# Kernel optimization log

Hardware: AMD Instinct MI355X
Metric: run time of the kernel (lower is better)

## Reference

```python
import jax, jax.numpy as jnp
import numpy as np


def _dct_last(x):
    # torch_dct along last axis: mirror-extend, forward-normalized FFT, sign(Re)*|X|
    L = x.shape[-1]
    arr = jnp.concatenate([x, x[..., ::-1]], axis=-1)
    X = jnp.fft.fft(arr, axis=-1, norm='forward')[..., :L]
    return jnp.abs(X) * jnp.sign(X.real)


def _dct_2d(x):
    row = _dct_last(x)
    col = _dct_last(jnp.swapaxes(row, -1, -2))
    return jnp.swapaxes(col, -1, -2)


def _dct_chan(x):
    # same transform along channel dim (axis 1)
    C = x.shape[1]
    arr = jnp.concatenate([x, x[:, ::-1]], axis=1)
    X = jnp.fft.fft(arr, axis=1, norm='forward')[:, :C]
    return jnp.abs(X) * jnp.sign(X.real)


def _idct_chan(x):
    # iDCT_Channel: shifted double-length spectrum -> ifft -> flipped real part
    B, C, H, W = x.shape
    v = jnp.arange(2 * C)
    shift = jnp.exp((-1j * 2.0 * jnp.pi * (C - 0.5) / (2 * C)) * v).astype(jnp.complex64)
    vi = x * (2.0 * C)
    flipneg = -vi[:, 1:][:, ::-1]                     # -flip(x[:,1:])
    full = jnp.concatenate([vi, jnp.zeros((B, 1, H, W), x.dtype), flipneg], axis=1)
    full = full.astype(jnp.complex64) * shift[None, :, None, None]
    xx = jnp.fft.ifft(full, axis=1)
    return xx[:, :C][:, ::-1].real


TOPK = 8
TOPK_CHANS = 8


def setup_inputs() -> dict:
    key = jax.random.key(0)
    k1, k2, k3, k4 = jax.random.split(key, 4)
    B, C, H, W = 4, 64, 256, 256
    red = 8
    return {
        'ip': jax.random.normal(k1, (B, C, H, W), dtype=jnp.float32),
        'fc1_w': jax.random.normal(k2, (C // red, C * TOPK), dtype=jnp.float32) * (1.0 / np.sqrt(C * TOPK)),
        'fc2_w': jax.random.normal(k3, (C, C // red), dtype=jnp.float32) * (1.0 / np.sqrt(C // red)),
        'conv_w': jax.random.normal(k4, (1, TOPK_CHANS, 3, 3), dtype=jnp.float32) * (1.0 / np.sqrt(TOPK_CHANS * 9)),
        'conv_b': jnp.zeros((1,), dtype=jnp.float32),
    }


def reference(ip, fc1_w, fc2_w, conv_w, conv_b):
    ip = ip.astype(jnp.float32)
    # channel-frequency attention
    ca = _dct_chan(ip)                                        # [B,C,H,W]
    ct = jnp.transpose(ca, (0, 2, 3, 1))                      # [B,H,W,C]
    topv = jax.lax.top_k(ct, TOPK_CHANS)[0]                   # [B,H,W,k]
    channel_topk = jnp.transpose(topv, (0, 3, 1, 2))          # [B,k,H,W]
    conv = jax.lax.conv_general_dilated(
        channel_topk, conv_w, (1, 1), 'SAME',
        dimension_numbers=('NCHW', 'OIHW', 'NCHW')) + conv_b[None, :, None, None]
    gate = jax.nn.sigmoid(conv)                               # [B,1,H,W]
    final = ca * gate
    x = _idct_chan(final).astype(jnp.float32)                 # [B,C,H,W]
    # spatial-DCT top-k channel gating MLP
    B, C = x.shape[0], x.shape[1]
    dct2 = _dct_2d(x).reshape(B, C, -1)                       # [B,C,H*W]
    topc = jax.lax.top_k(dct2, TOPK)[0].reshape(B, -1)        # [B,C*topk]
    h = jax.nn.relu(topc @ fc1_w.T)                           # [B,C//red]
    w = jax.nn.sigmoid(h @ fc2_w.T).reshape(B, C, 1, 1)       # [B,C,1,1]
    return x * w
```

## Files before the change

### kernel.cpp

```cpp
#include <hip/hip_runtime.h>
#include <hip/hip_bf16.h>
#include <math.h>

#define HW 65536
#define NCH 64
#define NB 4

typedef __attribute__((ext_vector_type(8))) short bf16x8;
typedef __attribute__((ext_vector_type(4))) float f32x4;
typedef __attribute__((ext_vector_type(8))) unsigned short u16x8;

__device__ inline unsigned short f2b(float f) {
  __hip_bfloat16 h = __float2bfloat16(f);
  return *(unsigned short*)&h;
}

__global__ void gen_tables(float* __restrict__ Mc, float* __restrict__ Nc,
                           unsigned short* __restrict__ Tb) {
  int i = blockIdx.x * 256 + threadIdx.x;
  const double PI = 3.14159265358979323846;
  if (i < 4096) {
    int k = i >> 6, c = i & 63;
    Mc[i] = (float)(cos(PI * (double)(k * (2 * c + 1)) / 128.0) / 64.0);
    Nc[i] = (c == 0) ? 1.0f
                     : (float)(2.0 * cos(PI * (double)(c * (2 * k + 1)) / 128.0));
  }
  {
    int n = i >> 8, k = i & 255;
    float v = (float)(cos(PI * (double)(n * (2 * k + 1)) / 512.0) / 256.0);
    Tb[i] = f2b(v);
  }
}

__global__ __launch_bounds__(256) void gemm64(
    const float* __restrict__ Ag, int lda, long long sAb,
    const float* __restrict__ Bg, int ldb, long long sBb,
    float* __restrict__ Cg, int ldc, long long sCb, int K,
    const float* __restrict__ gate, long long sGb) {
  __shared__ float As[16][68];
  __shared__ float Bs[16][68];
  const int tid = threadIdx.x;
  const int tx = tid & 15, ty = tid >> 4;
  const int bn = blockIdx.x, bm = blockIdx.y, bz = blockIdx.z;
  const float* Ab = Ag + bz * sAb + (long long)bm * 64 * lda;
  const float* Bp = Bg + bz * sBb;
  const long long n0 = (long long)bn * 64;
  const int bcol = tid & 63;
  const int brow = tid >> 6;
  const int acol = tid & 15;
  const int arow = tid >> 4;
  float g = 1.0f;
  if (gate) g = gate[bz * sGb + n0 + bcol];
  float acc[4][4] = {{0.f}};

  for (int k0 = 0; k0 < K; k0 += 16) {
#pragma unroll
    for (int i = 0; i < 4; i++) {
      int r = arow + 16 * i;
      As[acol][r] = Ab[(long long)r * lda + (k0 + acol)];
    }
#pragma unroll
    for (int i = 0; i < 4; i++) {
      int r = brow + 4 * i;
      Bs[r][bcol] = Bp[(long long)(k0 + r) * ldb + n0 + bcol] * g;
    }
    __syncthreads();
#pragma unroll
    for (int kk = 0; kk < 16; kk++) {
      float4 a4 = *(const float4*)&As[kk][ty * 4];
      float4 b4 = *(const float4*)&Bs[kk][tx * 4];
      float a[4] = {a4.x, a4.y, a4.z, a4.w};
      float b[4] = {b4.x, b4.y, b4.z, b4.w};
#pragma unroll
      for (int i = 0; i < 4; i++)
#pragma unroll
        for (int j = 0; j < 4; j++) acc[i][j] = fmaf(a[i], b[j], acc[i][j]);
    }
    __syncthreads();
  }
#pragma unroll
  for (int i = 0; i < 4; i++) {
    float4 o;
    o.x = acc[i][0]; o.y = acc[i][1]; o.z = acc[i][2]; o.w = acc[i][3];
    *(float4*)&Cg[bz * sCb + (long long)(bm * 64 + ty * 4 + i) * ldc + n0 +
                  tx * 4] = o;
  }
}

__global__ __launch_bounds__(256) void mfma_rowdct(
    const float* __restrict__ x, const unsigned short* __restrict__ Tb,
    unsigned short* __restrict__ Rt) {
  __shared__ unsigned short As[128][40];
  __shared__ unsigned short Bs[128][40];
  const int tid = threadIdx.x;
  const int m0 = blockIdx.y * 128;
  const int n0 = blockIdx.x * 128;
  const int wv = tid >> 6, lane = tid & 63;
  const int wr = wv >> 1, wc = wv & 1;
  const int l15 = lane & 15, kb = lane >> 4;
  const int srow = tid & 127, sseg = tid >> 7;
  f32x4 acc[4][4] = {};

  for (int k0 = 0; k0 < 256; k0 += 32) {
    {
      const float* p = x + (long long)(m0 + srow) * 256 + k0 + sseg * 8;
      float4 v0 = *(const float4*)p;
      float4 v1 = *(const float4*)(p + 4);
      u16x8 w;
      w[0] = f2b(v0.x); w[1] = f2b(v0.y); w[2] = f2b(v0.z); w[3] = f2b(v0.w);
      w[4] = f2b(v1.x); w[5] = f2b(v1.y); w[6] = f2b(v1.z); w[7] = f2b(v1.w);
      *(u16x8*)&As[srow][sseg * 8] = w;
    }
    *(u16x8*)&Bs[srow][sseg * 8] =
        *(const u16x8*)(Tb + (n0 + srow) * 256 + k0 + sseg * 8);
    __syncthreads();
    bf16x8 a[4], b[4];
#pragma unroll
    for (int mi = 0; mi < 4; mi++)
      a[mi] = *(const bf16x8*)&As[wr * 64 + mi * 16 + l15][kb * 8];
#pragma unroll
    for (int ni = 0; ni < 4; ni++)
      b[ni] = *(const bf16x8*)&Bs[wc * 64 + ni * 16 + l15][kb * 8];
#pragma unroll
    for (int mi = 0; mi < 4; mi++)
#pragma unroll
      for (int ni = 0; ni < 4; ni++)
        acc[mi][ni] = __builtin_amdgcn_mfma_f32_16x16x32_bf16(
            a[mi], b[ni], acc[mi][ni], 0, 0, 0);
    __syncthreads();
  }

  const int img = m0 >> 8;
  const int hb = (m0 & 255) + wr * 64 + kb * 4;
#pragma unroll
  for (int mi = 0; mi < 4; mi++) {
#pragma unroll
    for (int ni = 0; ni < 4; ni++) {
      int h = hb + mi * 16;
      int n = n0 + wc * 64 + ni * 16 + l15;
      ushort4 o;
      o.x = f2b(acc[mi][ni][0]); o.y = f2b(acc[mi][ni][1]);
      o.z = f2b(acc[mi][ni][2]); o.w = f2b(acc[mi][ni][3]);
      *(ushort4*)&Rt[(long long)img * 65536 + (long long)n * 256 + h] = o;
    }
  }
}

__global__ __launch_bounds__(256) void mfma_coldct_top8(
    const unsigned short* __restrict__ Tb, const unsigned short* __restrict__ Rt,
    float* __restrict__ top8out) {
  __shared__ unsigned short As[128][40];
  __shared__ unsigned short Bs[128][40];
  __shared__ float lists[256 * 8];
  const int tid = threadIdx.x;
  const int m0 = blockIdx.y * 128;
  const int n0 = blockIdx.x * 128;
  const int img = blockIdx.z;
  const int wv = tid >> 6, lane = tid & 63;
  const int wr = wv >> 1, wc = wv & 1;
  const int l15 = lane & 15, kb = lane >> 4;
  const int srow = tid & 127, sseg = tid >> 7;
  const unsigned short* Rb = Rt + (long long)img * 65536;
  f32x4 acc[4][4] = {};

  for (int k0 = 0; k0 < 256; k0 += 32) {
    *(u16x8*)&As[srow][sseg * 8] =
        *(const u16x8*)(Tb + (m0 + srow) * 256 + k0 + sseg * 8);
    *(u16x8*)&Bs[srow][sseg * 8] =
        *(const u16x8*)(Rb + (n0 + srow) * 256 + k0 + sseg * 8);
    __syncthreads();
    bf16x8 a[4], b[4];
#pragma unroll
    for (int mi = 0; mi < 4; mi++)
      a[mi] = *(const bf16x8*)&As[wr * 64 + mi * 16 + l15][kb * 8];
#pragma unroll
    for (int ni = 0; ni < 4; ni++)
      b[ni] = *(const bf16x8*)&Bs[wc * 64 + ni * 16 + l15][kb * 8];
#pragma unroll
    for (int mi = 0; mi < 4; mi++)
#pragma unroll
      for (int ni = 0; ni < 4; ni++)
        acc[mi][ni] = __builtin_amdgcn_mfma_f32_16x16x32_bf16(
            a[mi], b[ni], acc[mi][ni], 0, 0, 0);
    __syncthreads();
  }

  float t[8];
#pragma unroll
  for (int j = 0; j < 8; j++) t[j] = -INFINITY;
#pragma unroll
  for (int mi = 0; mi < 4; mi++)
#pragma unroll
    for (int ni = 0; ni < 4; ni++)
#pragma unroll
      for (int j = 0; j < 4; j++) {
        float v = acc[mi][ni][j];
#pragma unroll
        for (int q = 0; q < 8; q++) {
          if (v > t[q]) { float tmp = t[q]; t[q] = v; v = tmp; }
        }
      }
#pragma unroll
  for (int j = 0; j < 8; j++) lists[tid * 8 + j] = t[j];
  __syncthreads();
  for (int s = 128; s >= 1; s >>= 1) {
    if (tid < s) {
      int ii = 0, jj = 0;
      float out[8];
#pragma unroll
      for (int m = 0; m < 8; m++) {
        float av = lists[tid * 8 + ii];
        float bv = lists[(tid + s) * 8 + jj];
        bool ta = (av >= bv);
        out[m] = ta ? av : bv;
        ii += ta ? 1 : 0;
        jj += ta ? 0 : 1;
      }
#pragma unroll
      for (int m = 0; m < 8; m++) lists[tid * 8 + m] = out[m];
    }
    __syncthreads();
  }
  if (tid < 8) {
    long long idx = ((long long)img * gridDim.y + blockIdx.y) * gridDim.x +
                    blockIdx.x;
    top8out[idx * 8 + tid] = lists[tid];
  }
}

__global__ __launch_bounds__(256) void top8_chan(const float* __restrict__ ca,
                                                 float* __restrict__ ct) {
  int gidx = blockIdx.x * 256 + threadIdx.x;
  int b = gidx >> 16, p = gidx & 65535;
  const float* src = ca + (long long)b * NCH * HW + p;
  float t[8];
#pragma unroll
  for (int j = 0; j < 8; j++) t[j] = -INFINITY;
  for (int c = 0; c < NCH; c++) {
    float v = src[(long long)c * HW];
#pragma unroll
    for (int q = 0; q < 8; q++) {
      if (v > t[q]) { float tmp = t[q]; t[q] = v; v = tmp; }
    }
  }
  float* dst = ct + (long long)b * 8 * HW + p;
#pragma unroll
  for (int j = 0; j < 8; j++) dst[(long long)j * HW] = t[j];
}

__global__ __launch_bounds__(256) void conv_gate(const float* __restrict__ ct,
                                                 const float* __restrict__ cw,
                                                 const float* __restrict__ cbias,
                                                 float* __restrict__ gate) {
  int gidx = blockIdx.x * 256 + threadIdx.x;
  int b = gidx >> 16, p = gidx & 65535;
  int h = p >> 8, w = p & 255;
  float acc = cbias[0];
#pragma unroll
  for (int j = 0; j < 8; j++) {
    const float* base = ct + ((long long)b * 8 + j) * HW;
#pragma unroll
    for (int dy = 0; dy < 3; dy++) {
      int y = h + dy - 1;
      if ((unsigned)y < 256u) {
#pragma unroll
        for (int dx = 0; dx < 3; dx++) {
          int x = w + dx - 1;
          if ((unsigned)x < 256u)
            acc += base[y * 256 + x] * cw[j * 9 + dy * 3 + dx];
        }
      }
    }
  }
  gate[gidx] = 1.0f / (1.0f + expf(-acc));
}

__global__ void merge_top8(const float* __restrict__ lists,
                           float* __restrict__ topc) {
  int img = blockIdx.x * 64 + threadIdx.x;
  if (img >= 256) return;
  float t[8];
#pragma unroll
  for (int j = 0; j < 8; j++) t[j] = -INFINITY;
  for (int l = 0; l < 4; l++) {
#pragma unroll
    for (int m = 0; m < 8; m++) {
      float v = lists[(img * 4 + l) * 8 + m];
#pragma unroll
      for (int q = 0; q < 8; q++) {
        if (v > t[q]) { float tmp = t[q]; t[q] = v; v = tmp; }
      }
    }
  }
  int b = img >> 6, c = img & 63;
#pragma unroll
  for (int j = 0; j < 8; j++) topc[b * 512 + c * 8 + j] = t[j];
}

__global__ void mlp_kernel(const float* __restrict__ topc,
                           const float* __restrict__ fc1,
                           const float* __restrict__ fc2,
                           float* __restrict__ wout) {
  __shared__ float hbuf[32];
  int tid = threadIdx.x;
  if (tid < 32) {
    int b = tid >> 3, i = tid & 7;
    float acc = 0.f;
    for (int j = 0; j < 512; j++) acc += topc[b * 512 + j] * fc1[i * 512 + j];
    hbuf[tid] = fmaxf(acc, 0.f);
  }
  __syncthreads();
  int b = tid >> 6, c = tid & 63;
  float acc = 0.f;
#pragma unroll
  for (int i = 0; i < 8; i++) acc += hbuf[b * 8 + i] * fc2[c * 8 + i];
  wout[tid] = 1.0f / (1.0f + expf(-acc));
}

__global__ __launch_bounds__(256) void scale_out(float* __restrict__ out,
                                                 const float* __restrict__ wout) {
  long long i = ((long long)blockIdx.x * 256 + threadIdx.x) * 4;
  float4 v = *(float4*)&out[i];
  float s = wout[(int)(i >> 16)];
  v.x *= s; v.y *= s; v.z *= s; v.w *= s;
  *(float4*)&out[i] = v;
}

extern "C" void kernel_launch(void* const* d_in, const int* in_sizes, int n_in,
                              void* d_out, int out_size, void* d_ws,
                              size_t ws_size, hipStream_t stream) {
  (void)in_sizes; (void)n_in; (void)out_size; (void)ws_size;
  const float* ip  = (const float*)d_in[0];
  const float* fc1 = (const float*)d_in[1];
  const float* fc2 = (const float*)d_in[2];
  const float* cw  = (const float*)d_in[3];
  const float* cb  = (const float*)d_in[4];
  float* out = (float*)d_out;
  float* ws = (float*)d_ws;

  float* Mc     = ws;
  float* Nc     = ws + 4096;
  unsigned short* Tb = (unsigned short*)(ws + 8192);
  float* gateb  = ws + 139264;
  float* wfin   = ws + 401408;
  float* topc   = ws + 401664;
  float* listsb = ws + 403712;
  float* ca     = ws + 1048576;
  float* ct8    = ws + 1048576 + 16777216;

  const long long CHW = (long long)NCH * HW;

  gen_tables<<<256, 256, 0, stream>>>(Mc, Nc, Tb);

  gemm64<<<dim3(1024, 1, 4), 256, 0, stream>>>(
      Mc, 64, 0, ip, HW, CHW, ca, HW, CHW, 64, nullptr, 0);

  top8_chan<<<1024, 256, 0, stream>>>(ca, ct8);
  conv_gate<<<1024, 256, 0, stream>>>(ct8, cw, cb, gateb);

  gemm64<<<dim3(1024, 1, 4), 256, 0, stream>>>(
      Nc, 64, 0, ca, HW, CHW, out, HW, CHW, 64, gateb, HW);

  unsigned short* Rt = (unsigned short*)ca;
  mfma_rowdct<<<dim3(2, 512), 256, 0, stream>>>(out, Tb, Rt);

  mfma_coldct_top8<<<dim3(2, 2, 256), 256, 0, stream>>>(Tb, Rt, listsb);

  merge_top8<<<4, 64, 0, stream>>>(listsb, topc);
  mlp_kernel<<<1, 256, 0, stream>>>(topc, fc1, fc2, wfin);
  scale_out<<<16384, 256, 0, stream>>>(out, wfin);
}
```

Before: 321.0 us.

## Eliminate inverse channel DCT by applying gate directly to input

Because the channel gate depends only on (b,h,w), the inverse channel DCT of the gated spectrum reduces to the original input times the gate. The second 64x64 channel GEMM and its table are therefore removed. The gate multiply is folded into the row-DCT load and into the final scaling kernel, which now reads the input and gate instead of a stored intermediate. This saves a full read and write pass over the tensor. It relies on the forward and inverse transforms being exact inverses, treating abs times sign of the real part as equal to the real part.

```diff
diff --git a/kernel.cpp b/kernel.cpp
--- a/kernel.cpp
+++ b/kernel.cpp
@@ -15,15 +15,13 @@
   return *(unsigned short*)&h;
 }
 
-__global__ void gen_tables(float* __restrict__ Mc, float* __restrict__ Nc,
+__global__ void gen_tables(float* __restrict__ Mc,
                            unsigned short* __restrict__ Tb) {
   int i = blockIdx.x * 256 + threadIdx.x;
   const double PI = 3.14159265358979323846;
   if (i < 4096) {
     int k = i >> 6, c = i & 63;
     Mc[i] = (float)(cos(PI * (double)(k * (2 * c + 1)) / 128.0) / 64.0);
-    Nc[i] = (c == 0) ? 1.0f
-                     : (float)(2.0 * cos(PI * (double)(c * (2 * k + 1)) / 128.0));
   }
   {
     int n = i >> 8, k = i & 255;
@@ -87,9 +85,56 @@
   }
 }
 
+__global__ __launch_bounds__(256) void top8_chan(const float* __restrict__ ca,
+                                                 float* __restrict__ ct) {
+  int gidx = blockIdx.x * 256 + threadIdx.x;
+  int b = gidx >> 16, p = gidx & 65535;
+  const float* src = ca + (long long)b * NCH * HW + p;
+  float t[8];
+#pragma unroll
+  for (int j = 0; j < 8; j++) t[j] = -INFINITY;
+  for (int c = 0; c < NCH; c++) {
+    float v = src[(long long)c * HW];
+#pragma unroll
+    for (int q = 0; q < 8; q++) {
+      if (v > t[q]) { float tmp = t[q]; t[q] = v; v = tmp; }
+    }
+  }
+  float* dst = ct + (long long)b * 8 * HW + p;
+#pragma unroll
+  for (int j = 0; j < 8; j++) dst[(long long)j * HW] = t[j];
+}
+
+__global__ __launch_bounds__(256) void conv_gate(const float* __restrict__ ct,
+                                                 const float* __restrict__ cw,
+                                                 const float* __restrict__ cbias,
+                                                 float* __restrict__ gate) {
+  int gidx = blockIdx.x * 256 + threadIdx.x;
+  int b = gidx >> 16, p = gidx & 65535;
+  int h = p >> 8, w = p & 255;
+  float acc = cbias[0];
+#pragma unroll
+  for (int j = 0; j < 8; j++) {
+    const float* base = ct + ((long long)b * 8 + j) * HW;
+#pragma unroll
+    for (int dy = 0; dy < 3; dy++) {
+      int y = h + dy - 1;
+      if ((unsigned)y < 256u) {
+#pragma unroll
+        for (int dx = 0; dx < 3; dx++) {
+          int x = w + dx - 1;
+          if ((unsigned)x < 256u)
+            acc += base[y * 256 + x] * cw[j * 9 + dy * 3 + dx];
+        }
+      }
+    }
+  }
+  gate[gidx] = 1.0f / (1.0f + expf(-acc));
+}
+
 __global__ __launch_bounds__(256) void mfma_rowdct(
-    const float* __restrict__ x, const unsigned short* __restrict__ Tb,
-    unsigned short* __restrict__ Rt) {
+    const float* __restrict__ ip, const float* __restrict__ gateb,
+    const unsigned short* __restrict__ Tb, unsigned short* __restrict__ Rt) {
   __shared__ unsigned short As[128][40];
   __shared__ unsigned short Bs[128][40];
   const int tid = threadIdx.x;
@@ -103,12 +148,18 @@
 
   for (int k0 = 0; k0 < 256; k0 += 32) {
     {
-      const float* p = x + (long long)(m0 + srow) * 256 + k0 + sseg * 8;
-      float4 v0 = *(const float4*)p;
-      float4 v1 = *(const float4*)(p + 4);
+      const int r = m0 + srow;
+      const int h = r & 255;
+      const int b = r >> 14;
+      const float* p  = ip + (long long)r * 256 + k0 + sseg * 8;
+      const float* gp = gateb + ((long long)b << 16) + (h << 8) + k0 + sseg * 8;
+      float4 v0 = *(const float4*)p,  v1 = *(const float4*)(p + 4);
+      float4 g0 = *(const float4*)gp, g1 = *(const float4*)(gp + 4);
       u16x8 w;
-      w[0] = f2b(v0.x); w[1] = f2b(v0.y); w[2] = f2b(v0.z); w[3] = f2b(v0.w);
-      w[4] = f2b(v1.x); w[5] = f2b(v1.y); w[6] = f2b(v1.z); w[7] = f2b(v1.w);
+      w[0] = f2b(v0.x * g0.x); w[1] = f2b(v0.y * g0.y);
+      w[2] = f2b(v0.z * g0.z); w[3] = f2b(v0.w * g0.w);
+      w[4] = f2b(v1.x * g1.x); w[5] = f2b(v1.y * g1.y);
+      w[6] = f2b(v1.z * g1.z); w[7] = f2b(v1.w * g1.w);
       *(u16x8*)&As[srow][sseg * 8] = w;
     }
     *(u16x8*)&Bs[srow][sseg * 8] =
@@ -228,53 +279,6 @@
   }
 }
 
-__global__ __launch_bounds__(256) void top8_chan(const float* __restrict__ ca,
-                                                 float* __restrict__ ct) {
-  int gidx = blockIdx.x * 256 + threadIdx.x;
-  int b = gidx >> 16, p = gidx & 65535;
-  const float* src = ca + (long long)b * NCH * HW + p;
-  float t[8];
-#pragma unroll
-  for (int j = 0; j < 8; j++) t[j] = -INFINITY;
-  for (int c = 0; c < NCH; c++) {
-    float v = src[(long long)c * HW];
-#pragma unroll
-    for (int q = 0; q < 8; q++) {
-      if (v > t[q]) { float tmp = t[q]; t[q] = v; v = tmp; }
-    }
-  }
-  float* dst = ct + (long long)b * 8 * HW + p;
-#pragma unroll
-  for (int j = 0; j < 8; j++) dst[(long long)j * HW] = t[j];
-}
-
-__global__ __launch_bounds__(256) void conv_gate(const float* __restrict__ ct,
-                                                 const float* __restrict__ cw,
-                                                 const float* __restrict__ cbias,
-                                                 float* __restrict__ gate) {
-  int gidx = blockIdx.x * 256 + threadIdx.x;
-  int b = gidx >> 16, p = gidx & 65535;
-  int h = p >> 8, w = p & 255;
-  float acc = cbias[0];
-#pragma unroll
-  for (int j = 0; j < 8; j++) {
-    const float* base = ct + ((long long)b * 8 + j) * HW;
-#pragma unroll
-    for (int dy = 0; dy < 3; dy++) {
-      int y = h + dy - 1;
-      if ((unsigned)y < 256u) {
-#pragma unroll
-        for (int dx = 0; dx < 3; dx++) {
-          int x = w + dx - 1;
-          if ((unsigned)x < 256u)
-            acc += base[y * 256 + x] * cw[j * 9 + dy * 3 + dx];
-        }
-      }
-    }
-  }
-  gate[gidx] = 1.0f / (1.0f + expf(-acc));
-}
-
 __global__ void merge_top8(const float* __restrict__ lists,
                            float* __restrict__ topc) {
   int img = blockIdx.x * 64 + threadIdx.x;
@@ -317,12 +321,17 @@
   wout[tid] = 1.0f / (1.0f + expf(-acc));
 }
 
-__global__ __launch_bounds__(256) void scale_out(float* __restrict__ out,
-                                                 const float* __restrict__ wout) {
+__global__ __launch_bounds__(256) void final_scale(
+    const float* __restrict__ ip, const float* __restrict__ gateb,
+    const float* __restrict__ wfin, float* __restrict__ out) {
   long long i = ((long long)blockIdx.x * 256 + threadIdx.x) * 4;
-  float4 v = *(float4*)&out[i];
-  float s = wout[(int)(i >> 16)];
-  v.x *= s; v.y *= s; v.z *= s; v.w *= s;
+  int bc = (int)(i >> 16);
+  int b = bc >> 6;
+  int p = (int)(i & 65535);
+  float4 v = *(const float4*)&ip[i];
+  float4 g = *(const float4*)&gateb[((long long)b << 16) + p];
+  float s = wfin[bc];
+  v.x *= g.x * s; v.y *= g.y * s; v.z *= g.z * s; v.w *= g.w * s;
   *(float4*)&out[i] = v;
 }
 
@@ -339,7 +348,6 @@
   float* ws = (float*)d_ws;
 
   float* Mc     = ws;
-  float* Nc     = ws + 4096;
   unsigned short* Tb = (unsigned short*)(ws + 8192);
   float* gateb  = ws + 139264;
   float* wfin   = ws + 401408;
@@ -350,7 +358,7 @@
 
   const long long CHW = (long long)NCH * HW;
 
-  gen_tables<<<256, 256, 0, stream>>>(Mc, Nc, Tb);
+  gen_tables<<<256, 256, 0, stream>>>(Mc, Tb);
 
   gemm64<<<dim3(1024, 1, 4), 256, 0, stream>>>(
       Mc, 64, 0, ip, HW, CHW, ca, HW, CHW, 64, nullptr, 0);
@@ -358,15 +366,13 @@
   top8_chan<<<1024, 256, 0, stream>>>(ca, ct8);
   conv_gate<<<1024, 256, 0, stream>>>(ct8, cw, cb, gateb);
 
-  gemm64<<<dim3(1024, 1, 4), 256, 0, stream>>>(
-      Nc, 64, 0, ca, HW, CHW, out, HW, CHW, 64, gateb, HW);
-
   unsigned short* Rt = (unsigned short*)ca;
-  mfma_rowdct<<<dim3(2, 512), 256, 0, stream>>>(out, Tb, Rt);
+  mfma_rowdct<<<dim3(2, 512), 256, 0, stream>>>(ip, gateb, Tb, Rt);
 
   mfma_coldct_top8<<<dim3(2, 2, 256), 256, 0, stream>>>(Tb, Rt, listsb);
 
   merge_top8<<<4, 64, 0, stream>>>(listsb, topc);
   mlp_kernel<<<1, 256, 0, stream>>>(topc, fc1, fc2, wfin);
-  scale_out<<<16384, 256, 0, stream>>>(out, wfin);
-}
+
+  final_scale<<<16384, 256, 0, stream>>>(ip, gateb, wfin, out);
+}
```

After: 296.5 us. 7.6% less time.
